# Optimization experiments

Measured on AMD Instinct MI355X. Metric: run time of the kernel, lower is better.

Reference implementation:

```python
import jax, jax.numpy as jnp
import numpy as np

H = 8   # no_heads
D = 32  # c_hidden per head


def setup_inputs() -> dict:
    key = jax.random.key(0)
    ks = jax.random.split(key, 8)
    B, Q, K, C = 4, 1024, 1024, 256
    s = 0.02
    return {
        "q_x": jax.random.normal(ks[0], (B, Q, C), jnp.float32),
        "kv_x": jax.random.normal(ks[1], (B, K, C), jnp.float32),
        "mask_bias": jnp.zeros((B, 1, 1, K), jnp.float32),
        "pair_bias": jax.random.normal(ks[2], (B, H, Q, K), jnp.float32),
        "wq": jax.random.normal(ks[3], (H * D, C), jnp.float32) * s,
        "wk": jax.random.normal(ks[4], (H * D, C), jnp.float32) * s,
        "wv": jax.random.normal(ks[5], (H * D, C), jnp.float32) * s,
        "wg": jax.random.normal(ks[6], (H * D, C), jnp.float32) * s,
        "bg": jnp.zeros((H * D,), jnp.float32),
        "wo": jax.random.normal(ks[7], (C, H * D), jnp.float32) * s,
        "bo": jnp.zeros((C,), jnp.float32),
    }


def reference(q_x, kv_x, mask_bias, pair_bias, wq, wk, wv, wg, bg, wo, bo):
    B, Q, _ = q_x.shape
    K = kv_x.shape[1]
    # linear projections (no bias on q/k/v, as in OpenFold Attention)
    q = (q_x @ wq.T).reshape(B, Q, H, D) / jnp.sqrt(jnp.asarray(D, q_x.dtype))
    k = (kv_x @ wk.T).reshape(B, K, H, D)
    v = (kv_x @ wv.T).reshape(B, K, H, D)
    # scores + biases (mask bias broadcasts over heads/queries)
    a = jnp.einsum("bqhd,bkhd->bhqk", q, k) + mask_bias + pair_bias
    a = jax.nn.softmax(a, axis=-1)
    o = jnp.einsum("bhqk,bkhd->bqhd", a, v)  # [B,Q,H,D]
    # multiplicative gating from the query input
    g = jax.nn.sigmoid(q_x @ wg.T + bg).reshape(B, Q, H, D)
    o = o * g
    return (o.reshape(B, Q, H * D)) @ wo.T + bo
```

## Files before the change

### kernel.cpp

```cpp
#include <hip/hip_runtime.h>
#include <cstdint>
#include <cstddef>

typedef short bf16x8 __attribute__((ext_vector_type(8)));
typedef float f32x4 __attribute__((ext_vector_type(4)));
typedef unsigned short u16x4 __attribute__((ext_vector_type(4)));
typedef unsigned short u16x8 __attribute__((ext_vector_type(8)));

#define MFMA(a,b,c) __builtin_amdgcn_mfma_f32_16x16x32_bf16((a),(b),(c),0,0,0)

__device__ __forceinline__ unsigned short f2bf(float x){
  union { float f; unsigned u; } v; v.f = x;
  unsigned r = v.u + 0x7FFFu + ((v.u >> 16) & 1u);
  return (unsigned short)(r >> 16);
}
__device__ __forceinline__ float bf2f(unsigned short b){
  union { unsigned u; float f; } v; v.u = ((unsigned)b) << 16;
  return v.f;
}
__device__ __forceinline__ bf16x8 cvtld8(const float* p){
  f32x4 a = *(const f32x4*)p;
  f32x4 b = *(const f32x4*)(p + 4);
  bf16x8 r;
  r[0]=(short)f2bf(a.x); r[1]=(short)f2bf(a.y);
  r[2]=(short)f2bf(a.z); r[3]=(short)f2bf(a.w);
  r[4]=(short)f2bf(b.x); r[5]=(short)f2bf(b.y);
  r[6]=(short)f2bf(b.z); r[7]=(short)f2bf(b.w);
  return r;
}

__global__ __launch_bounds__(256) void wcvt_kernel(
    const float* __restrict__ wq, const float* __restrict__ wk,
    const float* __restrict__ wv, const float* __restrict__ wg,
    const float* __restrict__ wo, unsigned short* __restrict__ dst)
{
  const int which = blockIdx.x >> 5;
  const float* s = (which==0)?wq:(which==1)?wk:(which==2)?wv:(which==3)?wg:wo;
  const int off = (blockIdx.x & 31) * 2048 + threadIdx.x * 8;
  f32x4 a = *(const f32x4*)(s + off);
  f32x4 b = *(const f32x4*)(s + off + 4);
  u16x8 r;
  r[0]=f2bf(a.x); r[1]=f2bf(a.y); r[2]=f2bf(a.z); r[3]=f2bf(a.w);
  r[4]=f2bf(b.x); r[5]=f2bf(b.y); r[6]=f2bf(b.z); r[7]=f2bf(b.w);
  *(u16x8*)(dst + (size_t)which*65536 + off) = r;
}

__global__ __launch_bounds__(256,2) void proj_kernel(
    const float* __restrict__ q_x, const float* __restrict__ kv_x,
    const unsigned short* __restrict__ wb,
    const float* __restrict__ bg,
    unsigned short* __restrict__ qws, unsigned short* __restrict__ kws,
    unsigned short* __restrict__ vTws, unsigned short* __restrict__ gws)
{
  const int tid = threadIdx.x;
  const int w = tid >> 6, lane = tid & 63;
  const int c = lane & 15, qd = lane >> 4;
  const int side = blockIdx.x >> 8;
  const int rb = (blockIdx.x & 255) * 16;
  const float* X = side ? kv_x : q_x;
  const unsigned short* W0 = wb + (size_t)(side ? 1 : 0) * 65536;
  const unsigned short* W1 = wb + (size_t)(side ? 2 : 3) * 65536;
  const int hdw = w * 64;

  const f32x4 fz = {0.f,0.f,0.f,0.f};
  f32x4 acc[2][4];
  #pragma unroll
  for (int o=0;o<2;o++)
    #pragma unroll
    for (int mt=0;mt<4;mt++) acc[o][mt] = fz;

  #pragma unroll
  for (int ks = 0; ks < 8; ks++){
    const int ko = ks*32 + qd*8;
    bf16x8 bfrag = cvtld8(X + (size_t)(rb + c)*256 + ko);
    #pragma unroll
    for (int mt = 0; mt < 4; mt++){
      const int hd = hdw + mt*16 + c;
      bf16x8 a0 = *(const bf16x8*)(W0 + (size_t)hd*256 + ko);
      bf16x8 a1 = *(const bf16x8*)(W1 + (size_t)hd*256 + ko);
      acc[0][mt] = MFMA(a0, bfrag, acc[0][mt]);
      acc[1][mt] = MFMA(a1, bfrag, acc[1][mt]);
    }
  }

  const int row = rb + c;
  const int b = row >> 10, rr = row & 1023;
  #pragma unroll
  for (int mt = 0; mt < 4; mt++){
    const int hd0 = hdw + mt*16 + qd*4;
    const int h = hd0 >> 5, d0 = hd0 & 31;
    f32x4 v0 = acc[0][mt], v1 = acc[1][mt];
    if (side == 0){
      const float qs = 0.17677669529663687f;
      u16x4 oq = { f2bf(v0.x*qs), f2bf(v0.y*qs), f2bf(v0.z*qs), f2bf(v0.w*qs) };
      *(u16x4*)(qws + ((size_t)((b*8 + h)*1024 + rr))*32 + d0) = oq;
      f32x4 bg4 = *(const f32x4*)(bg + hd0);
      float g0 = 1.f/(1.f + exp2f(-1.44269504f*(v1.x + bg4.x)));
      float g1 = 1.f/(1.f + exp2f(-1.44269504f*(v1.y + bg4.y)));
      float g2 = 1.f/(1.f + exp2f(-1.44269504f*(v1.z + bg4.z)));
      float g3 = 1.f/(1.f + exp2f(-1.44269504f*(v1.w + bg4.w)));
      u16x4 og = { f2bf(g0), f2bf(g1), f2bf(g2), f2bf(g3) };
      *(u16x4*)(gws + ((size_t)((b*1024 + rr)*8 + h))*32 + d0) = og;
    } else {
      u16x4 ok = { f2bf(v0.x), f2bf(v0.y), f2bf(v0.z), f2bf(v0.w) };
      *(u16x4*)(kws + ((size_t)((b*8 + h)*1024 + rr))*32 + d0) = ok;
      size_t vb = ((size_t)((b*8 + h)*32 + d0))*1024 + rr;
      vTws[vb         ] = f2bf(v1.x);
      vTws[vb + 1024  ] = f2bf(v1.y);
      vTws[vb + 2048  ] = f2bf(v1.z);
      vTws[vb + 3072  ] = f2bf(v1.w);
    }
  }
}

__global__ __launch_bounds__(256,2) void attn_kernel(
    const float* __restrict__ pair_bias, const float* __restrict__ mask_bias,
    const unsigned short* __restrict__ qws, const unsigned short* __restrict__ kws,
    const unsigned short* __restrict__ vTws, const unsigned short* __restrict__ gws,
    unsigned short* __restrict__ ows)
{
  __shared__ __align__(16) unsigned char smem[67072];
  unsigned short* kT = (unsigned short*)smem;
  unsigned short* vT = (unsigned short*)(smem + 16384);
  unsigned short* pT = (unsigned short*)(smem + 33280);

  const int tid = threadIdx.x;
  const int w = tid >> 6, lane = tid & 63;
  const int c = lane & 15, qd = lane >> 4;
  const int bh = blockIdx.x >> 4, qb = blockIdx.x & 15;
  const int b  = bh >> 3, h = bh & 7;
  const int qrow = qb*64 + w*16 + c;

  const bf16x8 qf = *(const bf16x8*)(qws + ((size_t)bh*1024 + qrow)*32 + qd*8);
  const float* pbp = pair_bias + ((size_t)bh*1024 + qrow)*1024;
  const float* mbp = mask_bias + (size_t)b*1024;
  unsigned short* pTw = pT + w*4224;

  const f32x4 fz = {0.f,0.f,0.f,0.f};
  float m_i = -3.0e38f, l_i = 0.f;
  f32x4 accO0 = fz, accO1 = fz;

  for (int kc = 0; kc < 4; kc++){
    const int k0 = kc*256;
    #pragma unroll
    for (int i = 0; i < 4; i++){
      const int idx = i*256 + tid;
      const int plane = idx >> 8, key = idx & 255;
      u16x8 t8 = *(const u16x8*)(kws + ((size_t)bh*1024 + k0 + key)*32 + plane*8);
      *(u16x8*)(kT + idx*8) = t8;
    }
    #pragma unroll
    for (int i = 0; i < 4; i++){
      const int idx = i*256 + tid;
      const int d = idx >> 5, kch = idx & 31;
      u16x8 t8 = *(const u16x8*)(vTws + ((size_t)bh*32 + d)*1024 + k0 + kch*8);
      *(u16x8*)(vT + d*264 + kch*8) = t8;
    }
    __syncthreads();

    f32x4 sf[16];
    float cmax = -3.0e38f;
    #pragma unroll
    for (int t = 0; t < 16; t++){
      bf16x8 af = *(const bf16x8*)(kT + (qd*256 + t*16 + c)*8);
      f32x4 s = MFMA(af, qf, fz);
      f32x4 pb = *(const f32x4*)(pbp + k0 + t*16 + qd*4);
      f32x4 mb = *(const f32x4*)(mbp + k0 + t*16 + qd*4);
      s = (s + pb + mb) * 1.44269504f;
      sf[t] = s;
      cmax = fmaxf(cmax, fmaxf(fmaxf(s.x, s.y), fmaxf(s.z, s.w)));
    }
    cmax = fmaxf(cmax, __shfl_xor(cmax, 16));
    cmax = fmaxf(cmax, __shfl_xor(cmax, 32));
    const float m_new = fmaxf(m_i, cmax);
    const float alpha = exp2f(m_i - m_new);
    accO0 *= alpha; accO1 *= alpha;

    float rsum = 0.f;
    #pragma unroll
    for (int t = 0; t < 16; t++){
      f32x4 p;
      p.x = exp2f(sf[t].x - m_new);
      p.y = exp2f(sf[t].y - m_new);
      p.z = exp2f(sf[t].z - m_new);
      p.w = exp2f(sf[t].w - m_new);
      rsum += (p.x + p.y) + (p.z + p.w);
      u16x4 pk = { f2bf(p.x), f2bf(p.y), f2bf(p.z), f2bf(p.w) };
      *(u16x4*)(pTw + c*264 + t*16 + qd*4) = pk;
    }
    rsum += __shfl_xor(rsum, 16);
    rsum += __shfl_xor(rsum, 32);
    l_i = l_i*alpha + rsum;
    m_i = m_new;

    #pragma unroll
    for (int ks = 0; ks < 8; ks++){
      bf16x8 pf = *(const bf16x8*)(pTw + c*264 + ks*32 + qd*8);
      bf16x8 v0 = *(const bf16x8*)(vT + c*264 + ks*32 + qd*8);
      bf16x8 v1 = *(const bf16x8*)(vT + (16 + c)*264 + ks*32 + qd*8);
      accO0 = MFMA(v0, pf, accO0);
      accO1 = MFMA(v1, pf, accO1);
    }
    __syncthreads();
  }

  const float inv_l = 1.0f / l_i;
  const size_t obase = (((size_t)b*1024 + qrow)*8 + h)*32;
  {
    u16x4 g4 = *(const u16x4*)(gws + obase + qd*4);
    u16x4 o4 = { f2bf(accO0.x*inv_l*bf2f(g4[0])),
                 f2bf(accO0.y*inv_l*bf2f(g4[1])),
                 f2bf(accO0.z*inv_l*bf2f(g4[2])),
                 f2bf(accO0.w*inv_l*bf2f(g4[3])) };
    *(u16x4*)(ows + obase + qd*4) = o4;
  }
  {
    u16x4 g4 = *(const u16x4*)(gws + obase + 16 + qd*4);
    u16x4 o4 = { f2bf(accO1.x*inv_l*bf2f(g4[0])),
                 f2bf(accO1.y*inv_l*bf2f(g4[1])),
                 f2bf(accO1.z*inv_l*bf2f(g4[2])),
                 f2bf(accO1.w*inv_l*bf2f(g4[3])) };
    *(u16x4*)(ows + obase + 16 + qd*4) = o4;
  }
}

__global__ __launch_bounds__(256,2) void oproj_kernel(
    const unsigned short* __restrict__ ows, const unsigned short* __restrict__ wob,
    const float* __restrict__ bo, float* __restrict__ out)
{
  const int tid = threadIdx.x;
  const int w = tid >> 6, lane = tid & 63;
  const int c = lane & 15, qd = lane >> 4;
  const int row0 = blockIdx.x * 16;
  const int i0 = w * 64;

  const f32x4 fz = {0.f,0.f,0.f,0.f};
  f32x4 acc[4] = {fz, fz, fz, fz};
  #pragma unroll
  for (int ks = 0; ks < 8; ks++){
    const int ko = ks*32 + qd*8;
    bf16x8 bfrag = *(const bf16x8*)(ows + (size_t)(row0 + c)*256 + ko);
    #pragma unroll
    for (int mt = 0; mt < 4; mt++){
      bf16x8 afrag = *(const bf16x8*)(wob + (size_t)(i0 + mt*16 + c)*256 + ko);
      acc[mt] = MFMA(afrag, bfrag, acc[mt]);
    }
  }
  #pragma unroll
  for (int mt = 0; mt < 4; mt++){
    const int i = i0 + mt*16 + qd*4;
    f32x4 bo4 = *(const f32x4*)(bo + i);
    f32x4 r = acc[mt] + bo4;
    *(f32x4*)(out + (size_t)(row0 + c)*256 + i) = r;
  }
}

extern "C" void kernel_launch(void* const* d_in, const int* in_sizes, int n_in,
                              void* d_out, int out_size, void* d_ws, size_t ws_size,
                              hipStream_t stream) {
  const float* q_x       = (const float*)d_in[0];
  const float* kv_x      = (const float*)d_in[1];
  const float* mask_bias = (const float*)d_in[2];
  const float* pair_bias = (const float*)d_in[3];
  const float* wq        = (const float*)d_in[4];
  const float* wk        = (const float*)d_in[5];
  const float* wv        = (const float*)d_in[6];
  const float* wg        = (const float*)d_in[7];
  const float* bg        = (const float*)d_in[8];
  const float* wo        = (const float*)d_in[9];
  const float* bo        = (const float*)d_in[10];

  unsigned short* ws  = (unsigned short*)d_ws;
  unsigned short* qws  = ws;
  unsigned short* kws  = ws + (1u<<20);
  unsigned short* vTws = ws + 2*(1u<<20);
  unsigned short* gws  = ws + 3*(1u<<20);
  unsigned short* ows  = ws + 4*(1u<<20);
  unsigned short* wb   = ws + 5*(1u<<20);

  wcvt_kernel<<<160, 256, 0, stream>>>(wq, wk, wv, wg, wo, wb);
  proj_kernel<<<512, 256, 0, stream>>>(q_x, kv_x, wb, bg, qws, kws, vTws, gws);
  attn_kernel<<<512, 256, 0, stream>>>(pair_bias, mask_bias, qws, kws, vTws, gws, ows);
  oproj_kernel<<<256, 256, 0, stream>>>(ows, wb + 4*65536, bo, (float*)d_out);
}
```

Baseline: 256.4 us.

## Read K/V fragments directly from global memory and swizzle block order

Drops the shared-memory staging of K and V tiles and the block-wide barriers, so each wave loads its MFMA operands for K and V straight from global memory (relying on L2 and cache reuse). LDS use shrinks to the per-wave P buffer, which could raise occupancy. It also remaps block indices so consecutive blocks spread across (b,h) groups, changing L2 and XCD locality. The cost is redundant global loads of K/V, four times per block, one per wave.

```diff
diff --git a/kernel.cpp b/kernel.cpp
--- a/kernel.cpp
+++ b/kernel.cpp
@@ -119,21 +119,21 @@
     const unsigned short* __restrict__ vTws, const unsigned short* __restrict__ gws,
     unsigned short* __restrict__ ows)
 {
-  __shared__ __align__(16) unsigned char smem[67072];
-  unsigned short* kT = (unsigned short*)smem;
-  unsigned short* vT = (unsigned short*)(smem + 16384);
-  unsigned short* pT = (unsigned short*)(smem + 33280);
+  __shared__ __align__(16) unsigned short pT[4*4224];
 
   const int tid = threadIdx.x;
   const int w = tid >> 6, lane = tid & 63;
   const int c = lane & 15, qd = lane >> 4;
-  const int bh = blockIdx.x >> 4, qb = blockIdx.x & 15;
+  const int bid = (int)((blockIdx.x & 7) * 64 + (blockIdx.x >> 3));
+  const int bh = bid >> 4, qb = bid & 15;
   const int b  = bh >> 3, h = bh & 7;
   const int qrow = qb*64 + w*16 + c;
 
   const bf16x8 qf = *(const bf16x8*)(qws + ((size_t)bh*1024 + qrow)*32 + qd*8);
   const float* pbp = pair_bias + ((size_t)bh*1024 + qrow)*1024;
   const float* mbp = mask_bias + (size_t)b*1024;
+  const unsigned short* kbp = kws  + (size_t)bh*32768;
+  const unsigned short* vbp = vTws + (size_t)bh*32768;
   unsigned short* pTw = pT + w*4224;
 
   const f32x4 fz = {0.f,0.f,0.f,0.f};
@@ -142,27 +142,12 @@
 
   for (int kc = 0; kc < 4; kc++){
     const int k0 = kc*256;
-    #pragma unroll
-    for (int i = 0; i < 4; i++){
-      const int idx = i*256 + tid;
-      const int plane = idx >> 8, key = idx & 255;
-      u16x8 t8 = *(const u16x8*)(kws + ((size_t)bh*1024 + k0 + key)*32 + plane*8);
-      *(u16x8*)(kT + idx*8) = t8;
-    }
-    #pragma unroll
-    for (int i = 0; i < 4; i++){
-      const int idx = i*256 + tid;
-      const int d = idx >> 5, kch = idx & 31;
-      u16x8 t8 = *(const u16x8*)(vTws + ((size_t)bh*32 + d)*1024 + k0 + kch*8);
-      *(u16x8*)(vT + d*264 + kch*8) = t8;
-    }
-    __syncthreads();
 
     f32x4 sf[16];
     float cmax = -3.0e38f;
     #pragma unroll
     for (int t = 0; t < 16; t++){
-      bf16x8 af = *(const bf16x8*)(kT + (qd*256 + t*16 + c)*8);
+      bf16x8 af = *(const bf16x8*)(kbp + (size_t)(k0 + t*16 + c)*32 + qd*8);
       f32x4 s = MFMA(af, qf, fz);
       f32x4 pb = *(const f32x4*)(pbp + k0 + t*16 + qd*4);
       f32x4 mb = *(const f32x4*)(mbp + k0 + t*16 + qd*4);
@@ -196,12 +181,11 @@
     #pragma unroll
     for (int ks = 0; ks < 8; ks++){
       bf16x8 pf = *(const bf16x8*)(pTw + c*264 + ks*32 + qd*8);
-      bf16x8 v0 = *(const bf16x8*)(vT + c*264 + ks*32 + qd*8);
-      bf16x8 v1 = *(const bf16x8*)(vT + (16 + c)*264 + ks*32 + qd*8);
+      bf16x8 v0 = *(const bf16x8*)(vbp + (size_t)c*1024      + k0 + ks*32 + qd*8);
+      bf16x8 v1 = *(const bf16x8*)(vbp + (size_t)(16+c)*1024 + k0 + ks*32 + qd*8);
       accO0 = MFMA(v0, pf, accO0);
       accO1 = MFMA(v1, pf, accO1);
     }
-    __syncthreads();
   }
 
   const float inv_l = 1.0f / l_i;
```

New measurement: 277.9 us. 1.08x slower.
